# Kernel optimization log

Measured on AMD Instinct MI355X. Metric: run time of the kernel, lower is better.

Reference implementation:

```python
import jax, jax.numpy as jnp
import numpy as np

N_NODES = 50000
N_EDGES = 800000
D_IN = 512
D_HID = 64
D_OUT = 40


def setup_inputs() -> dict:
    key = jax.random.key(0)
    ks = jax.random.split(key, 8)
    x = jax.random.normal(ks[0], (N_NODES, D_IN), dtype=jnp.float32)
    edge_index = jax.random.randint(ks[1], (2, N_EDGES), 0, N_NODES, dtype=jnp.int32)
    w_mul = jax.random.uniform(ks[2], (N_EDGES,), dtype=jnp.float32)
    s1 = 1.0 / np.sqrt(D_IN)
    s2 = 1.0 / np.sqrt(D_HID)
    W1 = jax.random.uniform(ks[3], (D_IN, D_HID), minval=-s1, maxval=s1, dtype=jnp.float32)
    b1 = jax.random.uniform(ks[4], (D_HID,), minval=-s1, maxval=s1, dtype=jnp.float32)
    W2 = jax.random.uniform(ks[5], (D_HID, D_OUT), minval=-s2, maxval=s2, dtype=jnp.float32)
    b2 = jax.random.uniform(ks[6], (D_OUT,), minval=-s2, maxval=s2, dtype=jnp.float32)
    return {"x": x, "edge_index": edge_index, "w_mul": w_mul,
            "W1": W1, "b1": b1, "W2": W2, "b2": b2}


def _conv(h, src, dst, w_mul, W, b, n_nodes):
    # linear transform, then gather-scale-scatter-add (PyG aggr='add')
    h = h @ W + b                      # [N, d_out]
    msg = w_mul[:, None] * h[src]      # [E, d_out] gather + scale
    return jax.ops.segment_sum(msg, dst, num_segments=n_nodes)  # scatter-add


def reference(x, edge_index, w_mul, W1, b1, W2, b2):
    n_nodes = x.shape[0]
    src, dst = edge_index[0], edge_index[1]  # flow: source_to_target
    h = _conv(x, src, dst, w_mul, W1, b1, n_nodes)
    h = jax.nn.relu(h)
    h = _conv(h, src, dst, w_mul, W2, b2, n_nodes)
    return jax.nn.log_softmax(h, axis=1)
```

## Files before the change

### kernel.cpp

```cpp
#include <hip/hip_runtime.h>
#include <math.h>

#define D_IN  512
#define D_HID 64
#define D_OUT 40
#define CAP   64

typedef __attribute__((ext_vector_type(8))) short bf16x8;
typedef __attribute__((ext_vector_type(4))) float f32x4;

static __device__ __forceinline__ unsigned short f2bf(float f) {
    unsigned u = __float_as_uint(f);
    return (unsigned short)((u + 0x7FFF + ((u >> 16) & 1)) >> 16);
}
static __device__ __forceinline__ float bf2f(unsigned short h) {
    return __uint_as_float(((unsigned)h) << 16);
}

__global__ __launch_bounds__(256)
void prep_all(int* __restrict__ cursor, const float* __restrict__ W1,
              unsigned short* __restrict__ w1T, const float* __restrict__ W2,
              unsigned short* __restrict__ w2T, int N) {
    const int i = blockIdx.x * blockDim.x + threadIdx.x;
    if (i < N) cursor[i] = 0;
    const int j = i - N;
    if (j >= 0 && j < D_IN * D_HID) {
        const int k = j >> 6, col = j & 63;
        w1T[col * D_IN + k] = f2bf(W1[j]);
    }
    const int l = j - D_IN * D_HID;
    if (l >= 0 && l < 48 * D_HID) {
        const int col = l >> 6, k = l & 63;
        w2T[l] = (col < D_OUT) ? f2bf(W2[k * D_OUT + col]) : 0;
    }
}

__global__ __launch_bounds__(256)
void scatter_cap(const int* __restrict__ src, const int* __restrict__ dstA,
                 const float* __restrict__ wm, int* __restrict__ cursor,
                 unsigned* __restrict__ edges, int E, int N) {
    const int slice = (N + 7) >> 3;
    const int lo = (blockIdx.x & 7) * slice;
    const int hi = min(N, lo + slice);
    const int nChunk = gridDim.x >> 3;
    const int per = (E + nChunk - 1) / nChunk;
    const int beg = (blockIdx.x >> 3) * per;
    const int end = min(E, beg + per);
    for (int e = beg + threadIdx.x; e < end; e += blockDim.x) {
        const int d = dstA[e];
        if (d >= lo && d < hi) {
            const int pos = atomicAdd(&cursor[d], 1);
            if (pos < CAP)
                edges[(size_t)d * CAP + pos] =
                    ((unsigned)src[e] << 16) | (unsigned)f2bf(wm[e]);
        }
    }
}

__global__ __launch_bounds__(256)
void gemm1_mfma(const float* __restrict__ x, const unsigned short* __restrict__ w1T,
                const float* __restrict__ b1, unsigned short* __restrict__ h1, int N) {
    __shared__ unsigned char lds[16384];
    const int t = threadIdx.x;
    const int lane = t & 63;
    const int wv = t >> 6;
    const int nodeBase = blockIdx.x * 64;

    f32x4 acc[4];
#pragma unroll
    for (int cg = 0; cg < 4; ++cg) acc[cg] = (f32x4){0.f, 0.f, 0.f, 0.f};

    for (int k0 = 0; k0 < D_IN; k0 += 64) {
#pragma unroll
        for (int hh = 0; hh < 2; ++hh) {
            const int g = t + hh * 256;
            const int row = g >> 3, slot = g & 7;
            int gn = nodeBase + row; if (gn >= N) gn = N - 1;
            const float* sp = x + (size_t)gn * D_IN + k0 + slot * 8;
            const float4 a = *reinterpret_cast<const float4*>(sp);
            const float4 b = *reinterpret_cast<const float4*>(sp + 4);
            uint4 p;
            p.x = (unsigned)f2bf(a.x) | ((unsigned)f2bf(a.y) << 16);
            p.y = (unsigned)f2bf(a.z) | ((unsigned)f2bf(a.w) << 16);
            p.z = (unsigned)f2bf(b.x) | ((unsigned)f2bf(b.y) << 16);
            p.w = (unsigned)f2bf(b.z) | ((unsigned)f2bf(b.w) << 16);
            *reinterpret_cast<uint4*>(lds + row * 128 + ((slot << 4) ^ ((row & 7) << 4))) = p;
        }
#pragma unroll
        for (int hh = 0; hh < 2; ++hh) {
            const int g = t + hh * 256;
            const int col = g >> 3, slot = g & 7;
            const uint4 p = *reinterpret_cast<const uint4*>(w1T + (size_t)col * D_IN + k0 + slot * 8);
            *reinterpret_cast<uint4*>(lds + 8192 + col * 128 + ((slot << 4) ^ ((col & 7) << 4))) = p;
        }
        __syncthreads();

        const int fr = lane & 15;
        const int fc = lane >> 4;
#pragma unroll
        for (int s = 0; s < 2; ++s) {
            const int slot = s * 4 + fc;
            const int arow = wv * 16 + fr;
            const bf16x8 afrag = *reinterpret_cast<const bf16x8*>(
                lds + arow * 128 + ((slot << 4) ^ ((arow & 7) << 4)));
#pragma unroll
            for (int cg = 0; cg < 4; ++cg) {
                const int brow = cg * 16 + fr;
                const bf16x8 bfrag = *reinterpret_cast<const bf16x8*>(
                    lds + 8192 + brow * 128 + ((slot << 4) ^ ((brow & 7) << 4)));
                acc[cg] = __builtin_amdgcn_mfma_f32_16x16x32_bf16(afrag, bfrag, acc[cg], 0, 0, 0);
            }
        }
        __syncthreads();
    }

    const int fr = lane & 15;
    const int rq = lane >> 4;
#pragma unroll
    for (int cg = 0; cg < 4; ++cg) {
        const int col = cg * 16 + fr;
        const float bb = b1[col];
#pragma unroll
        for (int r = 0; r < 4; ++r) {
            const int node = nodeBase + wv * 16 + rq * 4 + r;
            if (node < N)
                h1[(size_t)node * D_HID + col] = f2bf(acc[cg][r] + bb);
        }
    }
}

__global__ __launch_bounds__(256)
void agg_hid(const unsigned short* __restrict__ h, const unsigned* __restrict__ edges,
             const int* __restrict__ count, unsigned short* __restrict__ agg1, int N) {
    const int lane = threadIdx.x & 63;
    const int n = (blockIdx.x * blockDim.x + threadIdx.x) >> 6;
    if (n >= N) return;
    const unsigned er = edges[(size_t)n * CAP + lane];
    const int cnt = min(count[n], CAP);
    float acc = 0.f;
    int j = 0;
    for (; j + 8 <= cnt; j += 8) {
        unsigned p[8];
#pragma unroll
        for (int u = 0; u < 8; ++u) p[u] = (unsigned)__shfl((int)er, j + u);
        float v[8];
#pragma unroll
        for (int u = 0; u < 8; ++u) v[u] = bf2f(h[(size_t)(p[u] >> 16) * D_HID + lane]);
#pragma unroll
        for (int u = 0; u < 8; ++u)
            acc += bf2f((unsigned short)(p[u] & 0xffff)) * v[u];
    }
    for (; j < cnt; ++j) {
        const unsigned p0 = (unsigned)__shfl((int)er, j);
        acc += bf2f((unsigned short)(p0 & 0xffff)) *
               bf2f(h[(size_t)(p0 >> 16) * D_HID + lane]);
    }
    agg1[(size_t)n * D_HID + lane] = f2bf(fmaxf(acc, 0.f));
}

__global__ __launch_bounds__(256)
void gemm2_mfma(const unsigned short* __restrict__ agg1,
                const unsigned short* __restrict__ w2T,
                const float* __restrict__ b2, unsigned short* __restrict__ h2, int N) {
    __shared__ unsigned char lds[8192 + 6144];
    const int t = threadIdx.x;
    const int lane = t & 63;
    const int wv = t >> 6;
    const int nodeBase = blockIdx.x * 64;

#pragma unroll
    for (int hh = 0; hh < 2; ++hh) {
        const int g = t + hh * 256;
        const int row = g >> 3, slot = g & 7;
        int gn = nodeBase + row; if (gn >= N) gn = N - 1;
        const uint4 p = *reinterpret_cast<const uint4*>(agg1 + (size_t)gn * D_HID + slot * 8);
        *reinterpret_cast<uint4*>(lds + row * 128 + ((slot << 4) ^ ((row & 7) << 4))) = p;
    }
    for (int g = t; g < 384; g += 256) {
        const int row = g >> 3, slot = g & 7;
        const uint4 p = *reinterpret_cast<const uint4*>(w2T + (size_t)row * D_HID + slot * 8);
        *reinterpret_cast<uint4*>(lds + 8192 + row * 128 + ((slot << 4) ^ ((row & 7) << 4))) = p;
    }
    __syncthreads();

    f32x4 acc[3];
#pragma unroll
    for (int cg = 0; cg < 3; ++cg) acc[cg] = (f32x4){0.f, 0.f, 0.f, 0.f};

    const int fr = lane & 15;
    const int fc = lane >> 4;
#pragma unroll
    for (int s = 0; s < 2; ++s) {
        const int slot = s * 4 + fc;
        const int arow = wv * 16 + fr;
        const bf16x8 afrag = *reinterpret_cast<const bf16x8*>(
            lds + arow * 128 + ((slot << 4) ^ ((arow & 7) << 4)));
#pragma unroll
        for (int cg = 0; cg < 3; ++cg) {
            const int brow = cg * 16 + fr;
            const bf16x8 bfrag = *reinterpret_cast<const bf16x8*>(
                lds + 8192 + brow * 128 + ((slot << 4) ^ ((brow & 7) << 4)));
            acc[cg] = __builtin_amdgcn_mfma_f32_16x16x32_bf16(afrag, bfrag, acc[cg], 0, 0, 0);
        }
    }

    const int rq = lane >> 4;
#pragma unroll
    for (int cg = 0; cg < 3; ++cg) {
        const int col = cg * 16 + fr;
        if (col < D_OUT) {
            const float bb = b2[col];
#pragma unroll
            for (int r = 0; r < 4; ++r) {
                const int node = nodeBase + wv * 16 + rq * 4 + r;
                if (node < N)
                    h2[(size_t)node * D_OUT + col] = f2bf(acc[cg][r] + bb);
            }
        }
    }
}

__global__ __launch_bounds__(256)
void agg40_lsm(const unsigned short* __restrict__ h2, const unsigned* __restrict__ edges,
               const int* __restrict__ count, float* __restrict__ out, int N) {
    const int lane = threadIdx.x & 63;
    const int col  = (lane < D_OUT) ? lane : 0;
    const int n = (blockIdx.x * blockDim.x + threadIdx.x) >> 6;
    if (n >= N) return;
    const unsigned er = edges[(size_t)n * CAP + lane];
    const int cnt = min(count[n], CAP);
    float acc = 0.f;
    int j = 0;
    for (; j + 8 <= cnt; j += 8) {
        unsigned p[8];
#pragma unroll
        for (int u = 0; u < 8; ++u) p[u] = (unsigned)__shfl((int)er, j + u);
        float v[8];
#pragma unroll
        for (int u = 0; u < 8; ++u) v[u] = bf2f(h2[(size_t)(p[u] >> 16) * D_OUT + col]);
#pragma unroll
        for (int u = 0; u < 8; ++u)
            acc += bf2f((unsigned short)(p[u] & 0xffff)) * v[u];
    }
    for (; j < cnt; ++j) {
        const unsigned p0 = (unsigned)__shfl((int)er, j);
        acc += bf2f((unsigned short)(p0 & 0xffff)) *
               bf2f(h2[(size_t)(p0 >> 16) * D_OUT + col]);
    }
    const float v = (lane < D_OUT) ? acc : -INFINITY;
    float m = v;
#pragma unroll
    for (int o = 32; o > 0; o >>= 1) m = fmaxf(m, __shfl_xor(m, o, 64));
    float s = (lane < D_OUT) ? __expf(v - m) : 0.f;
#pragma unroll
    for (int o = 32; o > 0; o >>= 1) s += __shfl_xor(s, o, 64);
    if (lane < D_OUT) out[(size_t)n * D_OUT + lane] = v - m - __logf(s);
}

extern "C" void kernel_launch(void* const* d_in, const int* in_sizes, int n_in,
                              void* d_out, int out_size, void* d_ws, size_t ws_size,
                              hipStream_t stream) {
    const float* x   = (const float*)d_in[0];
    const int*   ei  = (const int*)d_in[1];
    const float* wm  = (const float*)d_in[2];
    const float* W1  = (const float*)d_in[3];
    const float* b1  = (const float*)d_in[4];
    const float* W2  = (const float*)d_in[5];
    const float* b2  = (const float*)d_in[6];

    const int N = in_sizes[0] / D_IN;
    const int E = in_sizes[2];
    const int* srcIdx = ei;
    const int* dstIdx = ei + E;

    unsigned short* w1T    = (unsigned short*)d_ws;
    unsigned short* h1bf   = w1T + (size_t)D_HID * D_IN;
    unsigned short* agg1bf = h1bf + (size_t)N * D_HID;
    unsigned* edges        = (unsigned*)(agg1bf + (size_t)N * D_HID);
    int*   cursor          = (int*)(edges + (size_t)N * CAP);
    unsigned short* w2T    = (unsigned short*)(cursor + N);
    unsigned short* h2bf   = h1bf;
    float* out             = (float*)d_out;

    const int g1Blocks = (N + 63) / 64;
    const int prepWork = N + D_IN * D_HID + 48 * D_HID;

    prep_all<<<(prepWork + 255) / 256, 256, 0, stream>>>(cursor, W1, w1T, W2, w2T, N);
    scatter_cap<<<2048, 256, 0, stream>>>(srcIdx, dstIdx, wm, cursor, edges, E, N);
    gemm1_mfma<<<g1Blocks, 256, 0, stream>>>(x, w1T, b1, h1bf, N);
    agg_hid<<<(N * 64 + 255) / 256, 256, 0, stream>>>(h1bf, edges, cursor, agg1bf, N);
    gemm2_mfma<<<g1Blocks, 256, 0, stream>>>(agg1bf, w2T, b2, h2bf, N);
    agg40_lsm<<<(N * 64 + 255) / 256, 256, 0, stream>>>(h2bf, edges, cursor, out, N);
}
```

Measured before the change: 131.9 us.

## Fuse edge scatter and first GEMM into one launch; remap aggregation blocks by XCD slice

Merges the capped CSR scatter and the first MFMA GEMM into a single kernel. The first 1024 blocks do the scatter and the rest do the GEMM, so the two independent stages can run concurrently and one launch is removed. It also halves the scatter block count, which changes how the edge range is split into chunks. Both aggregation kernels remap block indices so that blocks with the same blockIdx mod 8 handle one contiguous node slice, matching the scatter's partition and likely aiming at L2 locality per XCD. The risks are load imbalance between the heterogeneous blocks and fewer blocks available for the scatter.

Result: faster. 116.4 us (-11.8%).

```diff
diff --git a/kernel.cpp b/kernel.cpp
--- a/kernel.cpp
+++ b/kernel.cpp
@@ -36,35 +36,37 @@
 }
 
 __global__ __launch_bounds__(256)
-void scatter_cap(const int* __restrict__ src, const int* __restrict__ dstA,
-                 const float* __restrict__ wm, int* __restrict__ cursor,
-                 unsigned* __restrict__ edges, int E, int N) {
-    const int slice = (N + 7) >> 3;
-    const int lo = (blockIdx.x & 7) * slice;
-    const int hi = min(N, lo + slice);
-    const int nChunk = gridDim.x >> 3;
-    const int per = (E + nChunk - 1) / nChunk;
-    const int beg = (blockIdx.x >> 3) * per;
-    const int end = min(E, beg + per);
-    for (int e = beg + threadIdx.x; e < end; e += blockDim.x) {
-        const int d = dstA[e];
-        if (d >= lo && d < hi) {
-            const int pos = atomicAdd(&cursor[d], 1);
-            if (pos < CAP)
-                edges[(size_t)d * CAP + pos] =
-                    ((unsigned)src[e] << 16) | (unsigned)f2bf(wm[e]);
-        }
-    }
-}
-
-__global__ __launch_bounds__(256)
-void gemm1_mfma(const float* __restrict__ x, const unsigned short* __restrict__ w1T,
-                const float* __restrict__ b1, unsigned short* __restrict__ h1, int N) {
+void fat1(const float* __restrict__ x, const unsigned short* __restrict__ w1T,
+          const float* __restrict__ b1, unsigned short* __restrict__ h1,
+          const int* __restrict__ src, const int* __restrict__ dstA,
+          const float* __restrict__ wm, int* __restrict__ cursor,
+          unsigned* __restrict__ edges, int E, int N, int sBlocks) {
     __shared__ unsigned char lds[16384];
     const int t = threadIdx.x;
+
+    if ((int)blockIdx.x < sBlocks) {
+        const int slice = (N + 7) >> 3;
+        const int lo = (blockIdx.x & 7) * slice;
+        const int hi = min(N, lo + slice);
+        const int nChunk = sBlocks >> 3;
+        const int per = (E + nChunk - 1) / nChunk;
+        const int beg = ((int)blockIdx.x >> 3) * per;
+        const int end = min(E, beg + per);
+        for (int e = beg + t; e < end; e += 256) {
+            const int d = dstA[e];
+            if (d >= lo && d < hi) {
+                const int pos = atomicAdd(&cursor[d], 1);
+                if (pos < CAP)
+                    edges[(size_t)d * CAP + pos] =
+                        ((unsigned)src[e] << 16) | (unsigned)f2bf(wm[e]);
+            }
+        }
+        return;
+    }
+
     const int lane = t & 63;
     const int wv = t >> 6;
-    const int nodeBase = blockIdx.x * 64;
+    const int nodeBase = ((int)blockIdx.x - sBlocks) * 64;
 
     f32x4 acc[4];
 #pragma unroll
@@ -133,7 +135,11 @@
 void agg_hid(const unsigned short* __restrict__ h, const unsigned* __restrict__ edges,
              const int* __restrict__ count, unsigned short* __restrict__ agg1, int N) {
     const int lane = threadIdx.x & 63;
-    const int n = (blockIdx.x * blockDim.x + threadIdx.x) >> 6;
+    const int wv   = (threadIdx.x >> 6);
+    const int slice = (N + 7) >> 3;
+    const int local = ((int)blockIdx.x >> 3) * 4 + wv;
+    if (local >= slice) return;
+    const int n = ((int)blockIdx.x & 7) * slice + local;
     if (n >= N) return;
     const unsigned er = edges[(size_t)n * CAP + lane];
     const int cnt = min(count[n], CAP);
@@ -225,7 +231,11 @@
                const int* __restrict__ count, float* __restrict__ out, int N) {
     const int lane = threadIdx.x & 63;
     const int col  = (lane < D_OUT) ? lane : 0;
-    const int n = (blockIdx.x * blockDim.x + threadIdx.x) >> 6;
+    const int wv   = (threadIdx.x >> 6);
+    const int slice = (N + 7) >> 3;
+    const int local = ((int)blockIdx.x >> 3) * 4 + wv;
+    if (local >= slice) return;
+    const int n = ((int)blockIdx.x & 7) * slice + local;
     if (n >= N) return;
     const unsigned er = edges[(size_t)n * CAP + lane];
     const int cnt = min(count[n], CAP);
@@ -283,12 +293,15 @@
     float* out             = (float*)d_out;
 
     const int g1Blocks = (N + 63) / 64;
+    const int sBlocks  = 1024;
     const int prepWork = N + D_IN * D_HID + 48 * D_HID;
+    const int slice = (N + 7) >> 3;
+    const int aggBlocks = ((slice + 3) / 4) * 8;
 
     prep_all<<<(prepWork + 255) / 256, 256, 0, stream>>>(cursor, W1, w1T, W2, w2T, N);
-    scatter_cap<<<2048, 256, 0, stream>>>(srcIdx, dstIdx, wm, cursor, edges, E, N);
-    gemm1_mfma<<<g1Blocks, 256, 0, stream>>>(x, w1T, b1, h1bf, N);
-    agg_hid<<<(N * 64 + 255) / 256, 256, 0, stream>>>(h1bf, edges, cursor, agg1bf, N);
+    fat1<<<sBlocks + g1Blocks, 256, 0, stream>>>(
+        x, w1T, b1, h1bf, srcIdx, dstIdx, wm, cursor, edges, E, N, sBlocks);
+    agg_hid<<<aggBlocks, 256, 0, stream>>>(h1bf, edges, cursor, agg1bf, N);
     gemm2_mfma<<<g1Blocks, 256, 0, stream>>>(agg1bf, w2T, b2, h2bf, N);
-    agg40_lsm<<<(N * 64 + 255) / 256, 256, 0, stream>>>(h2bf, edges, cursor, out, N);
-}
+    agg40_lsm<<<aggBlocks, 256, 0, stream>>>(h2bf, edges, cursor, out, N);
+}
```
